# Kernel tuning notes

Hardware: AMD Instinct MI355X
Metric: run time of the kernel (lower is better)

## Reference

```python
import jax, jax.numpy as jnp
from jax import lax
import numpy as np

PADDING = 1
STRIDE = 1


def setup_inputs() -> dict:
    key = jax.random.key(0)
    k1, k2 = jax.random.split(key)
    x = jax.random.normal(k1, (256, 224, 224), dtype=jnp.float32)       # [C, H, W]
    kernel = jax.random.normal(k2, (256, 256, 3, 3), dtype=jnp.float32)  # [O, C, kh, kw]
    return {"x": x, "kernel": kernel}


def reference(x, kernel):
    # Direct conv2d with zero padding and stride, equivalent to the
    # nested-loop torch implementation (cross-correlation, no bias).
    out = lax.conv_general_dilated(
        x[None],                      # [1, C, H, W]
        kernel,                       # [O, C, kh, kw]
        window_strides=(STRIDE, STRIDE),
        padding=[(PADDING, PADDING), (PADDING, PADDING)],
        dimension_numbers=("NCHW", "OIHW", "NCHW"),
    )
    return out[0]                     # [O, Hout, Wout]
```

## Files before the change

kernel.cpp:

```cpp
#include <hip/hip_runtime.h>
#include <hip/hip_bf16.h>
#include <stdint.h>

#define C_IN  256
#define C_OUT 256
#define H_IN  224
#define W_IN  224
#define HP    226
#define WP    226
#define NPIX  (H_IN * W_IN)
#define BM    256
#define BN    256
#define BK    64

typedef __attribute__((ext_vector_type(8))) short short8;
typedef __attribute__((ext_vector_type(4))) float f32x4;

__device__ __forceinline__ unsigned short f2bf(float f) {
    __hip_bfloat16 b = __float2bfloat16(f);
    return *(unsigned short*)&b;
}

__device__ __forceinline__ void gl_lds16(const unsigned short* g, unsigned short* l) {
    __builtin_amdgcn_global_load_lds(
        (const __attribute__((address_space(1))) unsigned int*)g,
        (__attribute__((address_space(3))) unsigned int*)l,
        16, 0, 0);
}

__global__ void prep_all(const float* __restrict__ x, const float* __restrict__ wk,
                         unsigned short* __restrict__ xp, unsigned short* __restrict__ wb) {
    int b = blockIdx.x;
    int t = threadIdx.x;
    if (b < 3584) {
        int ct = b & 3, wt = (b >> 2) & 3, h = b >> 4;
        int c0 = ct * 64, w0 = wt * 64;
        __shared__ float tile[64][65];
        int w   = t & 63;
        int cl0 = t >> 6;
        #pragma unroll
        for (int i = 0; i < 16; ++i) {
            int cl = i * 4 + cl0;
            float v = 0.f;
            if (w0 + w < W_IN)
                v = x[(size_t)(c0 + cl) * NPIX + (size_t)h * W_IN + w0 + w];
            tile[cl][w] = v;
        }
        __syncthreads();
        int wc = t >> 2;
        int cc = (t & 3) * 16;
        if (w0 + wc < W_IN) {
            uint32_t pk[8];
            #pragma unroll
            for (int j = 0; j < 8; ++j) {
                unsigned short lo = f2bf(tile[cc + 2 * j][wc]);
                unsigned short hi = f2bf(tile[cc + 2 * j + 1][wc]);
                pk[j] = (uint32_t)lo | ((uint32_t)hi << 16);
            }
            size_t base = ((size_t)(h + 1) * WP + (w0 + wc + 1)) * C_IN + c0 + cc;
            uint4* dst = (uint4*)(xp + base);
            dst[0] = make_uint4(pk[0], pk[1], pk[2], pk[3]);
            dst[1] = make_uint4(pk[4], pk[5], pk[6], pk[7]);
        }
        return;
    }
    if (b < 5888) {
        int idx = (b - 3584) * 256 + t;
        int c = idx & 255, o = (idx >> 8) & 255, p = idx >> 16;
        wb[((size_t)p * 256 + o) * 256 + c] = f2bf(wk[((size_t)o * 256 + c) * 9 + p]);
        return;
    }
    int i = (b - 5888) * 256 + t;
    uint4 z = make_uint4(0u, 0u, 0u, 0u);
    if (i < 7232) {
        ((uint4*)xp)[i] = z;
    } else if (i < 14464) {
        ((uint4*)(xp + (size_t)225 * WP * C_IN))[i - 7232] = z;
    } else if (i < 21632) {
        int j = i - 14464; int h = 1 + (j >> 5); int c4 = j & 31;
        ((uint4*)(xp + ((size_t)h * WP) * C_IN))[c4] = z;
    } else if (i < 28800) {
        int j = i - 21632; int h = 1 + (j >> 5); int c4 = j & 31;
        ((uint4*)(xp + ((size_t)h * WP + 225) * C_IN))[c4] = z;
    }
}


__launch_bounds__(512, 2)
__global__ void conv_gemm(const unsigned short* __restrict__ xp,
                          const unsigned short* __restrict__ wb,
                          float* __restrict__ out) {
    int nt = blockIdx.x;
    int n0 = nt * BN;
    int t  = threadIdx.x;
    int l  = t & 63, wv = t >> 6;

    __shared__ __align__(16) unsigned short lds[2 * 32768];

    int q8 = ((l & 7) ^ (l >> 3)) * 8;
    int rA = l >> 3;
    int offA0, offA1, offA2, offA3, offB0, offB1, offB2, offB3;
    {
        int r0 = (wv * 4 + 0) * 8 + rA;
        int r1 = (wv * 4 + 1) * 8 + rA;
        int r2 = (wv * 4 + 2) * 8 + rA;
        int r3 = (wv * 4 + 3) * 8 + rA;
        offA0 = r0 * C_IN + q8;
        offA1 = r1 * C_IN + q8;
        offA2 = r2 * C_IN + q8;
        offA3 = r3 * C_IN + q8;
        int nc0 = n0 + r0, nc1 = n0 + r1, nc2 = n0 + r2, nc3 = n0 + r3;
        int h0 = nc0 / W_IN, h1 = nc1 / W_IN, h2 = nc2 / W_IN, h3 = nc3 / W_IN;
        offB0 = (h0 * WP + (nc0 - h0 * W_IN)) * C_IN + q8;
        offB1 = (h1 * WP + (nc1 - h1 * W_IN)) * C_IN + q8;
        offB2 = (h2 * WP + (nc2 - h2 * W_IN)) * C_IN + q8;
        offB3 = (h3 * WP + (nc3 - h3 * W_IN)) * C_IN + q8;
    }

    int la = l & 15;
    int lk = l >> 4;
    int wr = wv >> 2;
    int wc = wv & 3;
    int mo = wr * 128;
    int no = wc * 64;
    int xq0 = ((0 * 4 + lk) ^ (la & 7)) * 8;
    int xq1 = ((1 * 4 + lk) ^ (la & 7)) * 8;

    f32x4 acc[8][4];
    #pragma unroll
    for (int i = 0; i < 8; ++i)
        #pragma unroll
        for (int j = 0; j < 4; ++j)
            acc[i][j] = f32x4{0.f, 0.f, 0.f, 0.f};

#define STAGE(BD, S) do {                                                    \
    int s_ = (S);                                                            \
    int p_ = s_ >> 2, cs_ = (s_ & 3) << 6;                                   \
    int kh_ = (p_ * 11) >> 5; int kw_ = p_ - 3 * kh_;                        \
    const unsigned short* aS_ = wb + p_ * 65536 + cs_;                       \
    const unsigned short* bS_ = xp + (kh_ * WP + kw_) * C_IN + cs_;          \
    gl_lds16(aS_ + offA0, &lds[(BD) * 32768 + (wv * 4 + 0) * 512]);          \
    gl_lds16(aS_ + offA1, &lds[(BD) * 32768 + (wv * 4 + 1) * 512]);          \
    gl_lds16(aS_ + offA2, &lds[(BD) * 32768 + (wv * 4 + 2) * 512]);          \
    gl_lds16(aS_ + offA3, &lds[(BD) * 32768 + (wv * 4 + 3) * 512]);          \
    gl_lds16(bS_ + offB0, &lds[(BD) * 32768 + 16384 + (wv * 4 + 0) * 512]);  \
    gl_lds16(bS_ + offB1, &lds[(BD) * 32768 + 16384 + (wv * 4 + 1) * 512]);  \
    gl_lds16(bS_ + offB2, &lds[(BD) * 32768 + 16384 + (wv * 4 + 2) * 512]);  \
    gl_lds16(bS_ + offB3, &lds[(BD) * 32768 + 16384 + (wv * 4 + 3) * 512]);  \
} while (0)

#define MFMA_HALF(BC, XQ) do {                                               \
    short8 af_[8], bf_[4];                                                   \
    _Pragma("unroll")                                                        \
    for (int i_ = 0; i_ < 8; ++i_)                                           \
        af_[i_] = *(const short8*)&lds[(BC) * 32768 + (mo + i_ * 16 + la) * BK + (XQ)]; \
    _Pragma("unroll")                                                        \
    for (int j_ = 0; j_ < 4; ++j_)                                           \
        bf_[j_] = *(const short8*)&lds[(BC) * 32768 + 16384 + (no + j_ * 16 + la) * BK + (XQ)]; \
    asm volatile("s_waitcnt lgkmcnt(0)" ::: "memory");                       \
    __builtin_amdgcn_sched_barrier(0);                                       \
    __builtin_amdgcn_s_setprio(1);                                           \
    _Pragma("unroll")                                                        \
    for (int i_ = 0; i_ < 8; ++i_)                                           \
        _Pragma("unroll")                                                    \
        for (int j_ = 0; j_ < 4; ++j_)                                       \
            acc[i_][j_] = __builtin_amdgcn_mfma_f32_16x16x32_bf16(           \
                af_[i_], bf_[j_], acc[i_][j_], 0, 0, 0);                     \
    __builtin_amdgcn_s_setprio(0);                                           \
} while (0)

#define BODY(BC, S, DO_STAGE) do {                                           \
    if (DO_STAGE) STAGE((BC) ^ 1, (S) + 1);                                  \
    asm volatile("s_waitcnt vmcnt(%0)" :: "i"((DO_STAGE) ? 8 : 0) : "memory"); \
    __builtin_amdgcn_sched_barrier(0);                                       \
    __builtin_amdgcn_s_barrier();                                            \
    __builtin_amdgcn_sched_barrier(0);                                       \
    MFMA_HALF(BC, xq0);                                                      \
    MFMA_HALF(BC, xq1);                                                      \
    asm volatile("s_waitcnt lgkmcnt(0)" ::: "memory");                       \
    __builtin_amdgcn_sched_barrier(0);                                       \
    __builtin_amdgcn_s_barrier();                                            \
    __builtin_amdgcn_sched_barrier(0);                                       \
} while (0)

    STAGE(0, 0);
    #pragma unroll 1
    for (int k = 0; k < 17; ++k) {
        BODY(0, 2 * k, 1);
        BODY(1, 2 * k + 1, 1);
    }
    BODY(0, 34, 1);
    BODY(1, 35, 0);

#undef BODY
#undef MFMA_HALF
#undef STAGE

    int ro = lk * 4;
    #pragma unroll
    for (int i = 0; i < 8; ++i) {
        #pragma unroll
        for (int j = 0; j < 4; ++j) {
            int oo = mo + i * 16 + ro;
            int nn = n0 + no + j * 16 + la;
            #pragma unroll
            for (int r = 0; r < 4; ++r)
                out[(size_t)(oo + r) * NPIX + nn] = acc[i][j][r];
        }
    }
}

__global__ void conv_naive(const float* __restrict__ x, const float* __restrict__ wk,
                           float* __restrict__ out) {
    int idx = blockIdx.x * 256 + threadIdx.x;
    int n = idx % NPIX;
    int o = idx / NPIX;
    int h = n / W_IN, w = n - (n / W_IN) * W_IN;
    float s = 0.f;
    for (int c = 0; c < C_IN; ++c) {
        const float* xc = x + (size_t)c * NPIX;
        const float* wc = wk + ((size_t)o * C_IN + c) * 9;
        #pragma unroll
        for (int kh = 0; kh < 3; ++kh) {
            int hh = h + kh - 1;
            if (hh < 0 || hh >= H_IN) continue;
            #pragma unroll
            for (int kw = 0; kw < 3; ++kw) {
                int ww = w + kw - 1;
                if (ww < 0 || ww >= W_IN) continue;
                s += xc[hh * W_IN + ww] * wc[kh * 3 + kw];
            }
        }
    }
    out[idx] = s;
}

extern "C" void kernel_launch(void* const* d_in, const int* in_sizes, int n_in,
                              void* d_out, int out_size, void* d_ws, size_t ws_size,
                              hipStream_t stream) {
    const float* x  = (const float*)d_in[0];
    const float* wk = (const float*)d_in[1];
    float* out = (float*)d_out;

    const size_t xp_elems = (size_t)HP * WP * C_IN;
    const size_t wb_elems = (size_t)9 * 256 * 256;
    const size_t need = (xp_elems + wb_elems) * 2;

    if (ws_size < need) {
        conv_naive<<<(C_OUT * NPIX) / 256, 256, 0, stream>>>(x, wk, out);
        return;
    }

    unsigned short* xp = (unsigned short*)d_ws;
    unsigned short* wb = xp + xp_elems;

    prep_all<<<3584 + 2304 + 113, 256, 0, stream>>>(x, wk, xp, wb);
    conv_gemm<<<196, 512, 0, stream>>>(xp, wb, out);
}
```

Before: 88.82 us.

## Interleave global-to-LDS staging with MFMA subgroups and remap blocks across XCDs

Splits each K-step's prefetch into four quarter-stages, two loads each for A or B halves. These are issued between four MFMA subgroups instead of all at the top, so global-to-LDS traffic overlaps compute more evenly. Fragment registers shrink because A fragments are loaded four at a time. Block IDs are also remapped so each XCD gets a contiguous range of output tiles, which should improve L2 locality for the overlapping input rows. The cost is more scheduling points and a changed LDS row assignment that has to stay consistent with the swizzle.

New measurement: 80.92 us. -8.9%, faster.

```diff
diff --git a/kernel.cpp b/kernel.cpp
--- a/kernel.cpp
+++ b/kernel.cpp
@@ -90,7 +90,9 @@
 __global__ void conv_gemm(const unsigned short* __restrict__ xp,
                           const unsigned short* __restrict__ wb,
                           float* __restrict__ out) {
-    int nt = blockIdx.x;
+    int bid = blockIdx.x;
+    int xcd = bid & 7, orig = bid >> 3;
+    int nt = (xcd < 4 ? xcd * 25 : 100 + (xcd - 4) * 24) + orig;
     int n0 = nt * BN;
     int t  = threadIdx.x;
     int l  = t & 63, wv = t >> 6;
@@ -99,22 +101,19 @@
 
     int q8 = ((l & 7) ^ (l >> 3)) * 8;
     int rA = l >> 3;
-    int offA0, offA1, offA2, offA3, offB0, offB1, offB2, offB3;
+    int rowLo = 16 * wv + rA;
+    int rowHi = rowLo + 8;
+    int offA00 = rowLo * C_IN + q8;
+    int offA01 = rowHi * C_IN + q8;
+    int offA10 = (128 + rowLo) * C_IN + q8;
+    int offA11 = (128 + rowHi) * C_IN + q8;
+    int offB00, offB01, offB10, offB11;
     {
-        int r0 = (wv * 4 + 0) * 8 + rA;
-        int r1 = (wv * 4 + 1) * 8 + rA;
-        int r2 = (wv * 4 + 2) * 8 + rA;
-        int r3 = (wv * 4 + 3) * 8 + rA;
-        offA0 = r0 * C_IN + q8;
-        offA1 = r1 * C_IN + q8;
-        offA2 = r2 * C_IN + q8;
-        offA3 = r3 * C_IN + q8;
-        int nc0 = n0 + r0, nc1 = n0 + r1, nc2 = n0 + r2, nc3 = n0 + r3;
-        int h0 = nc0 / W_IN, h1 = nc1 / W_IN, h2 = nc2 / W_IN, h3 = nc3 / W_IN;
-        offB0 = (h0 * WP + (nc0 - h0 * W_IN)) * C_IN + q8;
-        offB1 = (h1 * WP + (nc1 - h1 * W_IN)) * C_IN + q8;
-        offB2 = (h2 * WP + (nc2 - h2 * W_IN)) * C_IN + q8;
-        offB3 = (h3 * WP + (nc3 - h3 * W_IN)) * C_IN + q8;
+        int nc;
+        nc = n0 + rowLo;       { int h_ = nc / W_IN; offB00 = (h_ * WP + nc - h_ * W_IN) * C_IN + q8; }
+        nc = n0 + rowHi;       { int h_ = nc / W_IN; offB01 = (h_ * WP + nc - h_ * W_IN) * C_IN + q8; }
+        nc = n0 + 128 + rowLo; { int h_ = nc / W_IN; offB10 = (h_ * WP + nc - h_ * W_IN) * C_IN + q8; }
+        nc = n0 + 128 + rowHi; { int h_ = nc / W_IN; offB11 = (h_ * WP + nc - h_ * W_IN) * C_IN + q8; }
     }
 
     int la = l & 15;
@@ -123,8 +122,8 @@
     int wc = wv & 3;
     int mo = wr * 128;
     int no = wc * 64;
-    int xq0 = ((0 * 4 + lk) ^ (la & 7)) * 8;
-    int xq1 = ((1 * 4 + lk) ^ (la & 7)) * 8;
+    int xq0 = (lk ^ (la & 7)) * 8;
+    int xq1 = ((4 + lk) ^ (la & 7)) * 8;
 
     f32x4 acc[8][4];
     #pragma unroll
@@ -133,68 +132,83 @@
         for (int j = 0; j < 4; ++j)
             acc[i][j] = f32x4{0.f, 0.f, 0.f, 0.f};
 
-#define STAGE(BD, S) do {                                                    \
-    int s_ = (S);                                                            \
-    int p_ = s_ >> 2, cs_ = (s_ & 3) << 6;                                   \
-    int kh_ = (p_ * 11) >> 5; int kw_ = p_ - 3 * kh_;                        \
-    const unsigned short* aS_ = wb + p_ * 65536 + cs_;                       \
-    const unsigned short* bS_ = xp + (kh_ * WP + kw_) * C_IN + cs_;          \
-    gl_lds16(aS_ + offA0, &lds[(BD) * 32768 + (wv * 4 + 0) * 512]);          \
-    gl_lds16(aS_ + offA1, &lds[(BD) * 32768 + (wv * 4 + 1) * 512]);          \
-    gl_lds16(aS_ + offA2, &lds[(BD) * 32768 + (wv * 4 + 2) * 512]);          \
-    gl_lds16(aS_ + offA3, &lds[(BD) * 32768 + (wv * 4 + 3) * 512]);          \
-    gl_lds16(bS_ + offB0, &lds[(BD) * 32768 + 16384 + (wv * 4 + 0) * 512]);  \
-    gl_lds16(bS_ + offB1, &lds[(BD) * 32768 + 16384 + (wv * 4 + 1) * 512]);  \
-    gl_lds16(bS_ + offB2, &lds[(BD) * 32768 + 16384 + (wv * 4 + 2) * 512]);  \
-    gl_lds16(bS_ + offB3, &lds[(BD) * 32768 + 16384 + (wv * 4 + 3) * 512]);  \
+#define STAGEH(BD, S, H) do {                                                \
+    int s_ = (S), p_ = s_ >> 2, cs_ = (s_ & 3) << 6;                         \
+    if ((H) < 2) {                                                           \
+        const unsigned short* g_ = wb + p_ * 65536 + cs_;                    \
+        unsigned short* d_ = &lds[(BD) * 32768 + (H) * 8192 + wv * 1024];    \
+        gl_lds16(g_ + ((H) ? offA10 : offA00), d_);                          \
+        gl_lds16(g_ + ((H) ? offA11 : offA01), d_ + 512);                    \
+    } else {                                                                 \
+        int kh_ = (p_ * 11) >> 5, kw_ = p_ - 3 * kh_;                        \
+        const unsigned short* g_ = xp + (kh_ * WP + kw_) * C_IN + cs_;       \
+        unsigned short* d_ = &lds[(BD) * 32768 + 16384 + ((H) - 2) * 8192 + wv * 1024]; \
+        gl_lds16(g_ + ((H) == 3 ? offB10 : offB00), d_);                     \
+        gl_lds16(g_ + ((H) == 3 ? offB11 : offB01), d_ + 512);               \
+    }                                                                        \
 } while (0)
 
-#define MFMA_HALF(BC, XQ) do {                                               \
-    short8 af_[8], bf_[4];                                                   \
-    _Pragma("unroll")                                                        \
-    for (int i_ = 0; i_ < 8; ++i_)                                           \
-        af_[i_] = *(const short8*)&lds[(BC) * 32768 + (mo + i_ * 16 + la) * BK + (XQ)]; \
-    _Pragma("unroll")                                                        \
-    for (int j_ = 0; j_ < 4; ++j_)                                           \
-        bf_[j_] = *(const short8*)&lds[(BC) * 32768 + 16384 + (no + j_ * 16 + la) * BK + (XQ)]; \
-    asm volatile("s_waitcnt lgkmcnt(0)" ::: "memory");                       \
-    __builtin_amdgcn_sched_barrier(0);                                       \
+#define MFMAG(AF, BF, GOFF) do {                                             \
     __builtin_amdgcn_s_setprio(1);                                           \
     _Pragma("unroll")                                                        \
-    for (int i_ = 0; i_ < 8; ++i_)                                           \
+    for (int i_ = 0; i_ < 4; ++i_)                                           \
         _Pragma("unroll")                                                    \
         for (int j_ = 0; j_ < 4; ++j_)                                       \
-            acc[i_][j_] = __builtin_amdgcn_mfma_f32_16x16x32_bf16(           \
-                af_[i_], bf_[j_], acc[i_][j_], 0, 0, 0);                     \
+            acc[(GOFF) + i_][j_] = __builtin_amdgcn_mfma_f32_16x16x32_bf16(  \
+                AF[i_], BF[j_], acc[(GOFF) + i_][j_], 0, 0, 0);              \
     __builtin_amdgcn_s_setprio(0);                                           \
 } while (0)
 
-#define BODY(BC, S, DO_STAGE) do {                                           \
-    if (DO_STAGE) STAGE((BC) ^ 1, (S) + 1);                                  \
-    asm volatile("s_waitcnt vmcnt(%0)" :: "i"((DO_STAGE) ? 8 : 0) : "memory"); \
+#define HALF(BC, SS, DO_STAGE, VMSTR) do {                                   \
+    if (DO_STAGE) STAGEH(1 ^ (BC), SS, 0);                                   \
+    asm volatile("s_waitcnt " VMSTR ::: "memory");                           \
     __builtin_amdgcn_sched_barrier(0);                                       \
     __builtin_amdgcn_s_barrier();                                            \
     __builtin_amdgcn_sched_barrier(0);                                       \
-    MFMA_HALF(BC, xq0);                                                      \
-    MFMA_HALF(BC, xq1);                                                      \
+    short8 bf0_[4], bf1_[4], a_[4];                                          \
+    _Pragma("unroll")                                                        \
+    for (int j_ = 0; j_ < 4; ++j_)                                           \
+        bf0_[j_] = *(const short8*)&lds[(BC) * 32768 + 16384 + (no + j_ * 16 + la) * BK + xq0]; \
+    _Pragma("unroll")                                                        \
+    for (int i_ = 0; i_ < 4; ++i_)                                           \
+        a_[i_] = *(const short8*)&lds[(BC) * 32768 + (mo + i_ * 16 + la) * BK + xq0]; \
+    MFMAG(a_, bf0_, 0);                                                      \
+    if (DO_STAGE) STAGEH(1 ^ (BC), SS, 1);                                   \
+    _Pragma("unroll")                                                        \
+    for (int i_ = 0; i_ < 4; ++i_)                                           \
+        a_[i_] = *(const short8*)&lds[(BC) * 32768 + (mo + 64 + i_ * 16 + la) * BK + xq0]; \
+    MFMAG(a_, bf0_, 4);                                                      \
+    if (DO_STAGE) STAGEH(1 ^ (BC), SS, 2);                                   \
+    _Pragma("unroll")                                                        \
+    for (int j_ = 0; j_ < 4; ++j_)                                           \
+        bf1_[j_] = *(const short8*)&lds[(BC) * 32768 + 16384 + (no + j_ * 16 + la) * BK + xq1]; \
+    _Pragma("unroll")                                                        \
+    for (int i_ = 0; i_ < 4; ++i_)                                           \
+        a_[i_] = *(const short8*)&lds[(BC) * 32768 + (mo + i_ * 16 + la) * BK + xq1]; \
+    MFMAG(a_, bf1_, 0);                                                      \
+    if (DO_STAGE) STAGEH(1 ^ (BC), SS, 3);                                   \
+    _Pragma("unroll")                                                        \
+    for (int i_ = 0; i_ < 4; ++i_)                                           \
+        a_[i_] = *(const short8*)&lds[(BC) * 32768 + (mo + 64 + i_ * 16 + la) * BK + xq1]; \
+    MFMAG(a_, bf1_, 4);                                                      \
     asm volatile("s_waitcnt lgkmcnt(0)" ::: "memory");                       \
     __builtin_amdgcn_sched_barrier(0);                                       \
     __builtin_amdgcn_s_barrier();                                            \
     __builtin_amdgcn_sched_barrier(0);                                       \
 } while (0)
 
-    STAGE(0, 0);
+    STAGEH(0, 0, 0); STAGEH(0, 0, 1); STAGEH(0, 0, 2); STAGEH(0, 0, 3);
     #pragma unroll 1
     for (int k = 0; k < 17; ++k) {
-        BODY(0, 2 * k, 1);
-        BODY(1, 2 * k + 1, 1);
-    }
-    BODY(0, 34, 1);
-    BODY(1, 35, 0);
-
-#undef BODY
-#undef MFMA_HALF
-#undef STAGE
+        HALF(0, 2 * k + 1, 1, "vmcnt(2)");
+        HALF(1, 2 * k + 2, 1, "vmcnt(2)");
+    }
+    HALF(0, 35, 1, "vmcnt(2)");
+    HALF(1, 0, 0, "vmcnt(0)");
+
+#undef HALF
+#undef MFMAG
+#undef STAGEH
 
     int ro = lk * 4;
     #pragma unroll
```
